# Kernel tuning notes

Hardware: AMD Instinct MI355X
Metric: run time of the kernel (lower is better)

## Reference

```python
import jax, jax.numpy as jnp
import numpy as np

EPS = 1e-5
DN = ('NCHW', 'OIHW', 'NCHW')


def _conv(x, w):
    return jax.lax.conv_general_dilated(x, w, (1, 1), 'SAME', dimension_numbers=DN)


def _bn(x, g, b, m, v):
    # eval-mode batchnorm over channel axis 1
    inv = jax.lax.rsqrt(v + EPS)
    return (x - m[:, None, None]) * (g * inv)[:, None, None] + b[:, None, None]


def setup_inputs() -> dict:
    key = jax.random.key(0)
    ks = jax.random.split(key, 32)
    dim, mid, B, H, W = 256, 128, 4, 128, 128
    d = {}
    d['x'] = jax.random.normal(ks[0], (B, dim, H, W), dtype=jnp.float32)

    def bn_params(i, c):
        return (jax.random.uniform(ks[i], (c,), dtype=jnp.float32) + 0.5,
                jax.random.normal(ks[i + 1], (c,), dtype=jnp.float32) * 0.1,
                jax.random.normal(ks[i + 2], (c,), dtype=jnp.float32) * 0.1,
                jax.random.uniform(ks[i + 3], (c,), dtype=jnp.float32) + 0.5)

    d['w_p1'] = jax.random.normal(ks[1], (mid, dim, 3, 3), dtype=jnp.float32) * 0.02
    d['g_p1'], d['b_p1'], d['m_p1'], d['v_p1'] = bn_params(2, mid)
    d['w_p2'] = jax.random.normal(ks[6], (mid, dim, 3, 3), dtype=jnp.float32) * 0.02
    d['g_p2'], d['b_p2'], d['m_p2'], d['v_p2'] = bn_params(7, mid)
    d['w_c1'] = jax.random.normal(ks[11], (dim, mid, 3, 3), dtype=jnp.float32) * 0.02
    d['g_c1'], d['b_c1'], d['m_c1'], d['v_c1'] = bn_params(12, dim)
    d['w_c2'] = jax.random.normal(ks[16], (dim, dim, 1, 1), dtype=jnp.float32) * 0.02
    d['g_c2'], d['b_c2'], d['m_c2'], d['v_c2'] = bn_params(17, dim)
    d['w_p3'] = jax.random.normal(ks[21], (dim, dim, 3, 3), dtype=jnp.float32) * 0.02
    d['g_p3'], d['b_p3'], d['m_p3'], d['v_p3'] = bn_params(22, dim)
    return d


def reference(x,
              w_p1, g_p1, b_p1, m_p1, v_p1,
              w_p2, g_p2, b_p2, m_p2, v_p2,
              w_c1, g_c1, b_c1, m_c1, v_c1,
              w_c2, g_c2, b_c2, m_c2, v_c2,
              w_p3, g_p3, b_p3, m_p3, v_p3):
    # conv-bn-relu branches (dim -> 128)
    p1 = jax.nn.relu(_bn(_conv(x, w_p1), g_p1, b_p1, m_p1, v_p1))
    p2 = jax.nn.relu(_bn(_conv(x, w_p2), g_p2, b_p2, m_p2, v_p2))
    # corner pooling: 'top' = reverse cummax over H (axis 2),
    #                 'left' = reverse cummax over W (axis 3)
    cp1 = jax.lax.cummax(p1, axis=2, reverse=True)
    cp2 = jax.lax.cummax(p2, axis=3, reverse=True)
    bn1 = _bn(_conv(cp1 + cp2, w_c1), g_c1, b_c1, m_c1, v_c1)
    bn2 = _bn(_conv(x, w_c2), g_c2, b_c2, m_c2, v_c2)
    r = jax.nn.relu(bn1 + bn2)
    out = jax.nn.relu(_bn(_conv(r, w_p3), g_p3, b_p3, m_p3, v_p3))
    return out
```

## Files before the change

kernel.cpp:

```cpp
#include <hip/hip_runtime.h>
#include <math.h>

#define HH 128
#define WW 128
#define HWSZ (128*128)

typedef __attribute__((ext_vector_type(8))) short short8;
typedef __attribute__((ext_vector_type(4))) float float4v;

__device__ inline short f2bf(float f) {
  unsigned x = __float_as_uint(f);
  unsigned r = (x + 0x7fffu + ((x >> 16) & 1u)) >> 16;
  return (short)r;
}
__device__ inline float bf2f(unsigned short u) {
  return __uint_as_float(((unsigned)u) << 16);
}
__device__ inline int swz(int row, int g) {
  return row * 32 + ((g ^ ((row >> 1) & 3)) << 3);
}

__global__ __launch_bounds__(256) void xcvt_kernel(const float* __restrict__ x,
                                                   short* __restrict__ xbf) {
  __shared__ short tile[32 * 264];
  const int t = threadIdx.x;
  const int h = blockIdx.x, b = blockIdx.y;
  for (int wc = 0; wc < 4; wc++) {
    const int w0 = wc * 32;
    __syncthreads();
    #pragma unroll
    for (int coi = 0; coi < 8; coi++) {
      int ci = coi * 32 + (t >> 3);
      int wq = t & 7;
      float4v f = *(const float4v*)&x[((size_t)b * 256 + ci) * HWSZ + h * WW + w0 + wq * 4];
      tile[(wq * 4 + 0) * 264 + ci] = f2bf(f.x);
      tile[(wq * 4 + 1) * 264 + ci] = f2bf(f.y);
      tile[(wq * 4 + 2) * 264 + ci] = f2bf(f.z);
      tile[(wq * 4 + 3) * 264 + ci] = f2bf(f.w);
    }
    __syncthreads();
    #pragma unroll
    for (int pass = 0; pass < 4; pass++) {
      int wl = pass * 8 + (t >> 5);
      int ci8 = (t & 31) * 8;
      short8 v = *(const short8*)&tile[wl * 264 + ci8];
      *(short8*)&xbf[(((size_t)b * HH + h) * WW + w0 + wl) * 256 + ci8] = v;
    }
  }
}

__global__ void wcvt3_kernel(const float* __restrict__ w, const float* __restrict__ g,
                             const float* __restrict__ v, short* __restrict__ out,
                             int Cin, int CoutW, int co_off) {
  int idx = blockIdx.x * blockDim.x + threadIdx.x;
  int total = CoutW * Cin * 9;
  if (idx >= total) return;
  int t  = idx % 9;
  int ci = (idx / 9) % Cin;
  int co = idx / (9 * Cin);
  float s = g[co] * rsqrtf(v[co] + 1e-5f);
  out[((size_t)t * 256 + co_off + co) * Cin + ci] = f2bf(w[idx] * s);
}

__global__ void wcvt1_kernel(const float* __restrict__ w, const float* __restrict__ g,
                             const float* __restrict__ v, short* __restrict__ out,
                             int Cin, int CoutW) {
  int idx = blockIdx.x * blockDim.x + threadIdx.x;
  if (idx >= CoutW * Cin) return;
  int co = idx / Cin;
  float s = g[co] * rsqrtf(v[co] + 1e-5f);
  out[idx] = f2bf(w[idx] * s);
}

template<int CIN_A, bool PHASE_B, int SHIFT_MODE, bool SPLIT_OUT, bool OUT_F32>
__global__ __launch_bounds__(256, 2) void conv_mfma(
    const short* __restrict__ srcA, const short* __restrict__ xB,
    const short* __restrict__ wbA, const short* __restrict__ wbB,
    const float* __restrict__ g0, const float* __restrict__ b0,
    const float* __restrict__ m0, const float* __restrict__ v0,
    const float* __restrict__ g1, const float* __restrict__ b1,
    const float* __restrict__ m1, const float* __restrict__ v1,
    void* __restrict__ out0, void* __restrict__ out1)
{
  __shared__ short A_s[130 * 32];
  __shared__ short B_s[3 * 256 * 32];

  const int tid  = threadIdx.x;
  const int wave = tid >> 6;
  const int lane = tid & 63;
  const int wm = wave & 1;
  const int wn = wave >> 1;
  const int lr = lane & 15;
  const int lk = lane >> 4;

  const int h  = blockIdx.x & 127;
  const int b  = blockIdx.x >> 7;

  constexpr int ncA = CIN_A / 32;
  const int dystart = (h == 0) ? 1 : 0;
  const int dyend   = (h == HH - 1) ? 2 : 3;
  const int chunksA = (dyend - dystart) * ncA;
  const int total   = chunksA + (PHASE_B ? 8 : 0);

  float4v acc[4][8];
  #pragma unroll
  for (int i = 0; i < 4; i++)
    #pragma unroll
    for (int j = 0; j < 8; j++) acc[i][j] = (float4v)(0.0f);

  short8 rA[3], rB[12];
  const short* aRow = nullptr;
  const short* bBase = nullptr;
  bool curIsA = true;

  auto decode = [&](int t, const short*& ar, const short*& bb, bool& isA) {
    isA = (t < chunksA);
    if (isA) {
      int dy  = dystart + t / ncA;
      int ci0 = (t % ncA) * 32;
      ar = srcA + (((size_t)b * HH + (h + dy - 1)) * WW) * CIN_A + ci0;
      bb = wbA + ((size_t)(dy * 3) * 256) * CIN_A + ci0;
    } else {
      int ci0 = (t - chunksA) * 32;
      ar = xB + (((size_t)b * HH + h) * WW) * 256 + ci0;
      bb = wbB + ci0;
    }
  };

  auto loadRegs = [&](const short* ar, const short* bb, bool isA) {
    if (isA) {
      #pragma unroll
      for (int i = 0; i < 2; i++) {
        int idx = tid + i * 256;
        int w = (idx >> 2) - 1, q = idx & 3;
        rA[i] = ((unsigned)w < (unsigned)WW)
                  ? *(const short8*)(ar + (size_t)w * CIN_A + q * 8) : (short8)(0);
      }
      if (tid < 8) {
        int idx = tid + 512;
        int w = (idx >> 2) - 1, q = idx & 3;
        rA[2] = ((unsigned)w < (unsigned)WW)
                  ? *(const short8*)(ar + (size_t)w * CIN_A + q * 8) : (short8)(0);
      }
      #pragma unroll
      for (int i = 0; i < 12; i++) {
        int idx = tid + i * 256;
        int dx = idx >> 10, rem = idx & 1023;
        int co = rem >> 2, q = rem & 3;
        rB[i] = *(const short8*)(bb + (size_t)(dx * 256 + co) * CIN_A + q * 8);
      }
    } else {
      #pragma unroll
      for (int i = 0; i < 2; i++) {
        int idx = tid + i * 256;
        int wp = idx >> 2, q = idx & 3;
        rA[i] = *(const short8*)(ar + (size_t)wp * 256 + q * 8);
      }
      #pragma unroll
      for (int i = 0; i < 4; i++) {
        int idx = tid + i * 256;
        int co = idx >> 2, q = idx & 3;
        rB[i] = *(const short8*)(bb + (size_t)co * 256 + q * 8);
      }
    }
  };

  auto storeLDS = [&](bool isA) {
    if (isA) {
      #pragma unroll
      for (int i = 0; i < 2; i++) {
        int idx = tid + i * 256;
        *(short8*)&A_s[swz(idx >> 2, idx & 3)] = rA[i];
      }
      if (tid < 8) {
        int idx = tid + 512;
        *(short8*)&A_s[swz(idx >> 2, idx & 3)] = rA[2];
      }
      #pragma unroll
      for (int i = 0; i < 12; i++) {
        int idx = tid + i * 256;
        int dx = idx >> 10, rem = idx & 1023;
        *(short8*)&B_s[swz(dx * 256 + (rem >> 2), rem & 3)] = rB[i];
      }
    } else {
      #pragma unroll
      for (int i = 0; i < 2; i++) {
        int idx = tid + i * 256;
        *(short8*)&A_s[swz(idx >> 2, idx & 3)] = rA[i];
      }
      #pragma unroll
      for (int i = 0; i < 4; i++) {
        int idx = tid + i * 256;
        *(short8*)&B_s[swz(idx >> 2, idx & 3)] = rB[i];
      }
    }
  };

  decode(0, aRow, bBase, curIsA);
  loadRegs(aRow, bBase, curIsA);

  for (int t = 0; t < total; t++) {
    bool isA = curIsA;
    __syncthreads();
    storeLDS(isA);
    __syncthreads();
    if (t + 1 < total) {
      decode(t + 1, aRow, bBase, curIsA);
      loadRegs(aRow, bBase, curIsA);
    }
    const int ndx = isA ? 3 : 1;
    for (int dx = 0; dx < ndx; dx++) {
      short8 af[4];
      #pragma unroll
      for (int mi = 0; mi < 4; mi++)
        af[mi] = *(const short8*)&A_s[swz(wm * 64 + mi * 16 + lr + dx, lk)];
      #pragma unroll
      for (int ni = 0; ni < 8; ni++) {
        short8 bfr = *(const short8*)&B_s[swz(dx * 256 + wn * 128 + ni * 16 + lr, lk)];
        #pragma unroll
        for (int mi = 0; mi < 4; mi++)
          acc[mi][ni] = __builtin_amdgcn_mfma_f32_16x16x32_bf16(af[mi], bfr, acc[mi][ni], 0, 0, 0);
      }
    }
  }

  #pragma unroll
  for (int ni = 0; ni < 8; ni++) {
    int c = wn * 128 + ni * 16 + lr;
    float sh;
    if (SHIFT_MODE == 0) {
      float s = g0[c] * rsqrtf(v0[c] + 1e-5f);
      sh = b0[c] - m0[c] * s;
    } else if (SHIFT_MODE == 1) {
      int cc = c & 127;
      const float* gg = (c < 128) ? g0 : g1;
      const float* bb = (c < 128) ? b0 : b1;
      const float* mm = (c < 128) ? m0 : m1;
      const float* vv = (c < 128) ? v0 : v1;
      float s = gg[cc] * rsqrtf(vv[cc] + 1e-5f);
      sh = bb[cc] - mm[cc] * s;
    } else {
      float s0 = g0[c] * rsqrtf(v0[c] + 1e-5f);
      float s1 = g1[c] * rsqrtf(v1[c] + 1e-5f);
      sh = (b0[c] - m0[c] * s0) + (b1[c] - m1[c] * s1);
    }
    #pragma unroll
    for (int mi = 0; mi < 4; mi++) {
      int px = wm * 64 + mi * 16 + lk * 4;
      float4v v = acc[mi][ni];
      v.x = fmaxf(v.x + sh, 0.0f);
      v.y = fmaxf(v.y + sh, 0.0f);
      v.z = fmaxf(v.z + sh, 0.0f);
      v.w = fmaxf(v.w + sh, 0.0f);
      if (OUT_F32) {
        float* ob = (float*)out0;
        *(float4v*)(ob + ((size_t)b * 256 + c) * HWSZ + (size_t)h * WW + px) = v;
      } else if (SPLIT_OUT) {
        short* ob = (short*)((c < 128) ? out0 : out1);
        size_t base = (((size_t)b * HH + h) * WW + px) * 128 + (c & 127);
        ob[base      ] = f2bf(v.x);
        ob[base + 128 ] = f2bf(v.y);
        ob[base + 256 ] = f2bf(v.z);
        ob[base + 384 ] = f2bf(v.w);
      } else {
        short* ob = (short*)out0;
        size_t base = (((size_t)b * HH + h) * WW + px) * 256 + c;
        ob[base      ] = f2bf(v.x);
        ob[base + 256 ] = f2bf(v.y);
        ob[base + 512 ] = f2bf(v.z);
        ob[base + 768 ] = f2bf(v.w);
      }
    }
  }
}

__global__ void colscan_kernel(unsigned* __restrict__ p) {
  const int t = threadIdx.x;
  const int wl = t >> 6, cp = t & 63;
  const int w = blockIdx.x * 4 + wl;
  const int b = blockIdx.y;
  float m0 = -INFINITY, m1 = -INFINITY;
  for (int h = HH - 1; h >= 0; h--) {
    size_t idx = (((size_t)b * HH + h) * WW + w) * 64 + cp;
    unsigned u = p[idx];
    float f0 = bf2f((unsigned short)(u & 0xffff));
    float f1 = bf2f((unsigned short)(u >> 16));
    m0 = fmaxf(m0, f0);
    m1 = fmaxf(m1, f1);
    p[idx] = ((unsigned)(unsigned short)f2bf(m1) << 16) | (unsigned short)f2bf(m0);
  }
}

__global__ __launch_bounds__(256) void rowscan_add_kernel(
    const short* __restrict__ p2, short* __restrict__ p1) {
  __shared__ short pl[128 * 128];
  const int tid = threadIdx.x;
  const int hb = blockIdx.x;
  const int b  = blockIdx.y;
  const size_t base = (((size_t)b * HH + hb) * WW) * 128;

  #pragma unroll
  for (int i = 0; i < 8; i++) {
    int idx = tid + i * 256;
    *(short8*)&pl[idx * 8] = *(const short8*)(p2 + base + (size_t)idx * 8);
  }
  __syncthreads();
  if (tid < 128) {
    float m = -INFINITY;
    for (int w = WW - 1; w >= 0; w--) {
      int a = w * 128 + tid;
      m = fmaxf(m, bf2f((unsigned short)pl[a]));
      pl[a] = (short)f2bf(m);
    }
  }
  __syncthreads();
  #pragma unroll
  for (int i = 0; i < 8; i++) {
    int idx = tid + i * 256;
    short8 sv = *(const short8*)&pl[idx * 8];
    short8 ov = *(const short8*)(p1 + base + (size_t)idx * 8);
    short8 rv;
    #pragma unroll
    for (int j = 0; j < 8; j++)
      rv[j] = f2bf(bf2f((unsigned short)sv[j]) + bf2f((unsigned short)ov[j]));
    *(short8*)(p1 + base + (size_t)idx * 8) = rv;
  }
}

extern "C" void kernel_launch(void* const* d_in, const int* in_sizes, int n_in,
                              void* d_out, int out_size, void* d_ws, size_t ws_size,
                              hipStream_t stream) {
  const float* x    = (const float*)d_in[0];
  const float* w_p1 = (const float*)d_in[1];
  const float* g_p1 = (const float*)d_in[2];
  const float* b_p1 = (const float*)d_in[3];
  const float* m_p1 = (const float*)d_in[4];
  const float* v_p1 = (const float*)d_in[5];
  const float* w_p2 = (const float*)d_in[6];
  const float* g_p2 = (const float*)d_in[7];
  const float* b_p2 = (const float*)d_in[8];
  const float* m_p2 = (const float*)d_in[9];
  const float* v_p2 = (const float*)d_in[10];
  const float* w_c1 = (const float*)d_in[11];
  const float* g_c1 = (const float*)d_in[12];
  const float* b_c1 = (const float*)d_in[13];
  const float* m_c1 = (const float*)d_in[14];
  const float* v_c1 = (const float*)d_in[15];
  const float* w_c2 = (const float*)d_in[16];
  const float* g_c2 = (const float*)d_in[17];
  const float* b_c2 = (const float*)d_in[18];
  const float* m_c2 = (const float*)d_in[19];
  const float* v_c2 = (const float*)d_in[20];
  const float* w_p3 = (const float*)d_in[21];
  const float* g_p3 = (const float*)d_in[22];
  const float* b_p3 = (const float*)d_in[23];
  const float* m_p3 = (const float*)d_in[24];
  const float* v_p3 = (const float*)d_in[25];

  char* ws = (char*)d_ws;
  short* p1  = (short*)(ws + 0);
  short* p2  = (short*)(ws + 16777216);
  short* r   = (short*)(ws + 33554432);
  short* xbf = (short*)(ws + 67108864);
  short* wb12 = r;
  short* wbc1 = p2;
  short* wbc2 = (short*)(ws + 16777216 + 589824);
  short* wbp3 = p1;

  xcvt_kernel<<<dim3(128, 4), 256, 0, stream>>>(x, xbf);

  wcvt3_kernel<<<(128 * 256 * 9 + 255) / 256, 256, 0, stream>>>(w_p1, g_p1, v_p1, wb12, 256, 128, 0);
  wcvt3_kernel<<<(128 * 256 * 9 + 255) / 256, 256, 0, stream>>>(w_p2, g_p2, v_p2, wb12, 256, 128, 128);

  conv_mfma<256, false, 1, true, false><<<dim3(512), 256, 0, stream>>>(
      xbf, nullptr, wb12, nullptr,
      g_p1, b_p1, m_p1, v_p1, g_p2, b_p2, m_p2, v_p2, (void*)p1, (void*)p2);

  colscan_kernel<<<dim3(32, 4), 256, 0, stream>>>((unsigned*)p1);
  rowscan_add_kernel<<<dim3(128, 4), 256, 0, stream>>>(p2, p1);

  wcvt3_kernel<<<(256 * 128 * 9 + 255) / 256, 256, 0, stream>>>(w_c1, g_c1, v_c1, wbc1, 128, 256, 0);
  wcvt1_kernel<<<(256 * 256 + 255) / 256, 256, 0, stream>>>(w_c2, g_c2, v_c2, wbc2, 256, 256);

  conv_mfma<128, true, 2, false, false><<<dim3(512), 256, 0, stream>>>(
      p1, xbf, wbc1, wbc2,
      g_c1, b_c1, m_c1, v_c1, g_c2, b_c2, m_c2, v_c2, (void*)r, nullptr);

  wcvt3_kernel<<<(256 * 256 * 9 + 255) / 256, 256, 0, stream>>>(w_p3, g_p3, v_p3, wbp3, 256, 256, 0);

  conv_mfma<256, false, 0, false, true><<<dim3(512), 256, 0, stream>>>(
      r, nullptr, wbp3, nullptr,
      g_p3, b_p3, m_p3, v_p3, nullptr, nullptr, nullptr, nullptr, d_out, nullptr);
}
```

Measured before the change: 427.7 us.

## Stream conv weights from global in fragment order and stage only activations in LDS

Weight conversion kernels now write weights pre-permuted into the per-lane MFMA fragment order, grouped by 32-channel chunk and tap. The conv kernel loads its B fragments directly from global or L2 into registers instead of staging all weights in LDS. Per channel chunk it stages the three needed input rows (zero-padded at the borders) in LDS once and loops over all 9 taps. This removes B LDS traffic and shrinks shared memory, but it drops the register prefetch double-buffering, so global weight-load latency sits on the MFMA path. The column scan is also rewritten to load tiles into LDS, scan there, and write back with vector accesses instead of strided per-element global traffic.

```diff
diff --git a/kernel.cpp b/kernel.cpp
--- a/kernel.cpp
+++ b/kernel.cpp
@@ -47,6 +47,13 @@
       *(short8*)&xbf[(((size_t)b * HH + h) * WW + w0 + wl) * 256 + ci8] = v;
     }
   }
+}
+
+__device__ inline int co_perm_idx(int co ) {
+  int half = co >> 7;
+  int cl = co & 127;
+  int ni = cl >> 4, lr = cl & 15;
+  return half * 128 + lr * 8 + ni;
 }
 
 __global__ void wcvt3_kernel(const float* __restrict__ w, const float* __restrict__ g,
@@ -59,7 +66,9 @@
   int ci = (idx / 9) % Cin;
   int co = idx / (9 * Cin);
   float s = g[co] * rsqrtf(v[co] + 1e-5f);
-  out[((size_t)t * 256 + co_off + co) * Cin + ci] = f2bf(w[idx] * s);
+  int gco = co_off + co;
+  size_t o = (((size_t)(ci >> 5) * 9 + t) * 256 + co_perm_idx(gco)) * 32 + (ci & 31);
+  out[o] = f2bf(w[idx] * s);
 }
 
 __global__ void wcvt1_kernel(const float* __restrict__ w, const float* __restrict__ g,
@@ -67,12 +76,14 @@
                              int Cin, int CoutW) {
   int idx = blockIdx.x * blockDim.x + threadIdx.x;
   if (idx >= CoutW * Cin) return;
+  int ci = idx % Cin;
   int co = idx / Cin;
   float s = g[co] * rsqrtf(v[co] + 1e-5f);
-  out[idx] = f2bf(w[idx] * s);
-}
-
-template<int CIN_A, bool PHASE_B, int SHIFT_MODE, bool SPLIT_OUT, bool OUT_F32>
+  size_t o = ((size_t)(ci >> 5) * 256 + co_perm_idx(co)) * 32 + (ci & 31);
+  out[o] = f2bf(w[idx] * s);
+}
+
+template<int CIN_A, int NB, int SHIFT_MODE, bool SPLIT_OUT, bool OUT_F32>
 __global__ __launch_bounds__(256, 2) void conv_mfma(
     const short* __restrict__ srcA, const short* __restrict__ xB,
     const short* __restrict__ wbA, const short* __restrict__ wbB,
@@ -82,8 +93,7 @@
     const float* __restrict__ m1, const float* __restrict__ v1,
     void* __restrict__ out0, void* __restrict__ out1)
 {
-  __shared__ short A_s[130 * 32];
-  __shared__ short B_s[3 * 256 * 32];
+  __shared__ short A_s[3 * 130 * 32];
 
   const int tid  = threadIdx.x;
   const int wave = tid >> 6;
@@ -97,10 +107,6 @@
   const int b  = blockIdx.x >> 7;
 
   constexpr int ncA = CIN_A / 32;
-  const int dystart = (h == 0) ? 1 : 0;
-  const int dyend   = (h == HH - 1) ? 2 : 3;
-  const int chunksA = (dyend - dystart) * ncA;
-  const int total   = chunksA + (PHASE_B ? 8 : 0);
 
   float4v acc[4][8];
   #pragma unroll
@@ -108,119 +114,69 @@
     #pragma unroll
     for (int j = 0; j < 8; j++) acc[i][j] = (float4v)(0.0f);
 
-  short8 rA[3], rB[12];
-  const short* aRow = nullptr;
-  const short* bBase = nullptr;
-  bool curIsA = true;
-
-  auto decode = [&](int t, const short*& ar, const short*& bb, bool& isA) {
-    isA = (t < chunksA);
+  for (int ch = 0; ch < ncA + NB; ch++) {
+    const bool isA = (ch < ncA);
+    __syncthreads();
     if (isA) {
-      int dy  = dystart + t / ncA;
-      int ci0 = (t % ncA) * 32;
-      ar = srcA + (((size_t)b * HH + (h + dy - 1)) * WW) * CIN_A + ci0;
-      bb = wbA + ((size_t)(dy * 3) * 256) * CIN_A + ci0;
-    } else {
-      int ci0 = (t - chunksA) * 32;
-      ar = xB + (((size_t)b * HH + h) * WW) * 256 + ci0;
-      bb = wbB + ci0;
-    }
-  };
-
-  auto loadRegs = [&](const short* ar, const short* bb, bool isA) {
-    if (isA) {
-      #pragma unroll
-      for (int i = 0; i < 2; i++) {
-        int idx = tid + i * 256;
-        int w = (idx >> 2) - 1, q = idx & 3;
-        rA[i] = ((unsigned)w < (unsigned)WW)
-                  ? *(const short8*)(ar + (size_t)w * CIN_A + q * 8) : (short8)(0);
-      }
-      if (tid < 8) {
-        int idx = tid + 512;
-        int w = (idx >> 2) - 1, q = idx & 3;
-        rA[2] = ((unsigned)w < (unsigned)WW)
-                  ? *(const short8*)(ar + (size_t)w * CIN_A + q * 8) : (short8)(0);
-      }
-      #pragma unroll
-      for (int i = 0; i < 12; i++) {
-        int idx = tid + i * 256;
-        int dx = idx >> 10, rem = idx & 1023;
-        int co = rem >> 2, q = rem & 3;
-        rB[i] = *(const short8*)(bb + (size_t)(dx * 256 + co) * CIN_A + q * 8);
+      const int ci0 = ch * 32;
+      for (int g = tid; g < 1560; g += 256) {
+        int dy  = g / 520;
+        int rem = g - dy * 520;
+        int wp = rem >> 2, q = rem & 3;
+        int gw = wp - 1;
+        int gh = h + dy - 1;
+        short8 val = (short8)(0);
+        if ((unsigned)gh < (unsigned)HH && (unsigned)gw < (unsigned)WW)
+          val = *(const short8*)(srcA + (((size_t)b * HH + gh) * WW + gw) * CIN_A + ci0 + q * 8);
+        *(short8*)&A_s[swz(dy * 130 + wp, q)] = val;
       }
     } else {
+      const int ci0 = (ch - ncA) * 32;
+      for (int g = tid; g < 512; g += 256) {
+        int wp = g >> 2, q = g & 3;
+        short8 val = *(const short8*)(xB + (((size_t)b * HH + h) * WW + wp) * 256 + ci0 + q * 8);
+        *(short8*)&A_s[swz(wp, q)] = val;
+      }
+    }
+    __syncthreads();
+
+    if (isA) {
+      const short* bch = wbA + ((size_t)ch * 9) * 256 * 32 + (wn * 128 + lr * 8) * 32 + lk * 8;
       #pragma unroll
-      for (int i = 0; i < 2; i++) {
-        int idx = tid + i * 256;
-        int wp = idx >> 2, q = idx & 3;
-        rA[i] = *(const short8*)(ar + (size_t)wp * 256 + q * 8);
-      }
-      #pragma unroll
-      for (int i = 0; i < 4; i++) {
-        int idx = tid + i * 256;
-        int co = idx >> 2, q = idx & 3;
-        rB[i] = *(const short8*)(bb + (size_t)co * 256 + q * 8);
-      }
-    }
-  };
-
-  auto storeLDS = [&](bool isA) {
-    if (isA) {
-      #pragma unroll
-      for (int i = 0; i < 2; i++) {
-        int idx = tid + i * 256;
-        *(short8*)&A_s[swz(idx >> 2, idx & 3)] = rA[i];
-      }
-      if (tid < 8) {
-        int idx = tid + 512;
-        *(short8*)&A_s[swz(idx >> 2, idx & 3)] = rA[2];
-      }
-      #pragma unroll
-      for (int i = 0; i < 12; i++) {
-        int idx = tid + i * 256;
-        int dx = idx >> 10, rem = idx & 1023;
-        *(short8*)&B_s[swz(dx * 256 + (rem >> 2), rem & 3)] = rB[i];
+      for (int tap = 0; tap < 9; tap++) {
+        const short* bp = bch + (size_t)tap * 256 * 32;
+        short8 bfr[8];
+        #pragma unroll
+        for (int ni = 0; ni < 8; ni++)
+          bfr[ni] = *(const short8*)(bp + ni * 32);
+        const int dy = tap / 3, dx = tap % 3;
+        const int rowbase = dy * 130 + dx;
+        short8 af[4];
+        #pragma unroll
+        for (int mi = 0; mi < 4; mi++)
+          af[mi] = *(const short8*)&A_s[swz(rowbase + wm * 64 + mi * 16 + lr, lk)];
+        #pragma unroll
+        for (int ni = 0; ni < 8; ni++)
+          #pragma unroll
+          for (int mi = 0; mi < 4; mi++)
+            acc[mi][ni] = __builtin_amdgcn_mfma_f32_16x16x32_bf16(af[mi], bfr[ni], acc[mi][ni], 0, 0, 0);
       }
     } else {
+      const int cb = ch - ncA;
+      const short* bp = wbB + ((size_t)cb * 256 + wn * 128 + lr * 8) * 32 + lk * 8;
+      short8 bfr[8];
       #pragma unroll
-      for (int i = 0; i < 2; i++) {
-        int idx = tid + i * 256;
-        *(short8*)&A_s[swz(idx >> 2, idx & 3)] = rA[i];
-      }
-      #pragma unroll
-      for (int i = 0; i < 4; i++) {
-        int idx = tid + i * 256;
-        *(short8*)&B_s[swz(idx >> 2, idx & 3)] = rB[i];
-      }
-    }
-  };
-
-  decode(0, aRow, bBase, curIsA);
-  loadRegs(aRow, bBase, curIsA);
-
-  for (int t = 0; t < total; t++) {
-    bool isA = curIsA;
-    __syncthreads();
-    storeLDS(isA);
-    __syncthreads();
-    if (t + 1 < total) {
-      decode(t + 1, aRow, bBase, curIsA);
-      loadRegs(aRow, bBase, curIsA);
-    }
-    const int ndx = isA ? 3 : 1;
-    for (int dx = 0; dx < ndx; dx++) {
+      for (int ni = 0; ni < 8; ni++)
+        bfr[ni] = *(const short8*)(bp + ni * 32);
       short8 af[4];
       #pragma unroll
       for (int mi = 0; mi < 4; mi++)
-        af[mi] = *(const short8*)&A_s[swz(wm * 64 + mi * 16 + lr + dx, lk)];
+        af[mi] = *(const short8*)&A_s[swz(wm * 64 + mi * 16 + lr, lk)];
       #pragma unroll
-      for (int ni = 0; ni < 8; ni++) {
-        short8 bfr = *(const short8*)&B_s[swz(dx * 256 + wn * 128 + ni * 16 + lr, lk)];
+      for (int ni = 0; ni < 8; ni++)
         #pragma unroll
         for (int mi = 0; mi < 4; mi++)
-          acc[mi][ni] = __builtin_amdgcn_mfma_f32_16x16x32_bf16(af[mi], bfr, acc[mi][ni], 0, 0, 0);
-      }
+          acc[mi][ni] = __builtin_amdgcn_mfma_f32_16x16x32_bf16(af[mi], bfr[ni], acc[mi][ni], 0, 0, 0);
     }
   }
 
@@ -274,20 +230,35 @@
   }
 }
 
-__global__ void colscan_kernel(unsigned* __restrict__ p) {
-  const int t = threadIdx.x;
-  const int wl = t >> 6, cp = t & 63;
-  const int w = blockIdx.x * 4 + wl;
-  const int b = blockIdx.y;
-  float m0 = -INFINITY, m1 = -INFINITY;
-  for (int h = HH - 1; h >= 0; h--) {
-    size_t idx = (((size_t)b * HH + h) * WW + w) * 64 + cp;
-    unsigned u = p[idx];
-    float f0 = bf2f((unsigned short)(u & 0xffff));
-    float f1 = bf2f((unsigned short)(u >> 16));
-    m0 = fmaxf(m0, f0);
-    m1 = fmaxf(m1, f1);
-    p[idx] = ((unsigned)(unsigned short)f2bf(m1) << 16) | (unsigned short)f2bf(m0);
+__global__ __launch_bounds__(256) void colscan_kernel(short* __restrict__ p) {
+  __shared__ short pl[128 * 2 * 128];
+  const int tid = threadIdx.x;
+  const int w0 = blockIdx.x * 2;
+  const int b  = blockIdx.y;
+  #pragma unroll
+  for (int i = 0; i < 16; i++) {
+    int g = tid + i * 256;
+    int hh = g >> 5; int rem = g & 31; int wl = rem >> 4; int c8 = rem & 15;
+    *(short8*)&pl[g * 8] =
+      *(const short8*)(p + (((size_t)b * HH + hh) * WW + w0 + wl) * 128 + c8 * 8);
+  }
+  __syncthreads();
+  {
+    int wl = tid >> 7, c = tid & 127;
+    float m = -INFINITY;
+    for (int hh = HH - 1; hh >= 0; hh--) {
+      int a = hh * 256 + wl * 128 + c;
+      m = fmaxf(m, bf2f((unsigned short)pl[a]));
+      pl[a] = (short)f2bf(m);
+    }
+  }
+  __syncthreads();
+  #pragma unroll
+  for (int i = 0; i < 16; i++) {
+    int g = tid + i * 256;
+    int hh = g >> 5; int rem = g & 31; int wl = rem >> 4; int c8 = rem & 15;
+    *(short8*)(p + (((size_t)b * HH + hh) * WW + w0 + wl) * 128 + c8 * 8) =
+      *(const short8*)&pl[g * 8];
   }
 }
 
@@ -372,23 +343,23 @@
   wcvt3_kernel<<<(128 * 256 * 9 + 255) / 256, 256, 0, stream>>>(w_p1, g_p1, v_p1, wb12, 256, 128, 0);
   wcvt3_kernel<<<(128 * 256 * 9 + 255) / 256, 256, 0, stream>>>(w_p2, g_p2, v_p2, wb12, 256, 128, 128);
 
-  conv_mfma<256, false, 1, true, false><<<dim3(512), 256, 0, stream>>>(
+  conv_mfma<256, 0, 1, true, false><<<dim3(512), 256, 0, stream>>>(
       xbf, nullptr, wb12, nullptr,
       g_p1, b_p1, m_p1, v_p1, g_p2, b_p2, m_p2, v_p2, (void*)p1, (void*)p2);
 
-  colscan_kernel<<<dim3(32, 4), 256, 0, stream>>>((unsigned*)p1);
+  colscan_kernel<<<dim3(64, 4), 256, 0, stream>>>(p1);
   rowscan_add_kernel<<<dim3(128, 4), 256, 0, stream>>>(p2, p1);
 
   wcvt3_kernel<<<(256 * 128 * 9 + 255) / 256, 256, 0, stream>>>(w_c1, g_c1, v_c1, wbc1, 128, 256, 0);
   wcvt1_kernel<<<(256 * 256 + 255) / 256, 256, 0, stream>>>(w_c2, g_c2, v_c2, wbc2, 256, 256);
 
-  conv_mfma<128, true, 2, false, false><<<dim3(512), 256, 0, stream>>>(
+  conv_mfma<128, 8, 2, false, false><<<dim3(512), 256, 0, stream>>>(
       p1, xbf, wbc1, wbc2,
       g_c1, b_c1, m_c1, v_c1, g_c2, b_c2, m_c2, v_c2, (void*)r, nullptr);
 
   wcvt3_kernel<<<(256 * 256 * 9 + 255) / 256, 256, 0, stream>>>(w_p3, g_p3, v_p3, wbp3, 256, 256, 0);
 
-  conv_mfma<256, false, 0, false, true><<<dim3(512), 256, 0, stream>>>(
+  conv_mfma<256, 0, 0, false, true><<<dim3(512), 256, 0, stream>>>(
       r, nullptr, wbp3, nullptr,
       g_p3, b_p3, m_p3, v_p3, nullptr, nullptr, nullptr, nullptr, d_out, nullptr);
 }
```

Result: slower. 644.9 us (+50.8%).
